# Kernel optimization log

Hardware: AMD Instinct MI355X
Metric: run time of the kernel (lower is better)

Reference implementation:

```python
import jax, jax.numpy as jnp
import numpy as np

T, B, D, H = 512, 64, 512, 512  # seq_len, batch, input_size, hidden_size


def setup_inputs() -> dict:
    key = jax.random.key(0)
    ks = jax.random.split(key, 7)
    s = jnp.float32(0.05)  # keep gates out of saturation
    return {
        "x": jax.random.normal(ks[0], (T, B, D), jnp.float32),
        "Wi_l0": jax.random.normal(ks[1], (2, 4 * H, D), jnp.float32) * s,
        "Wh_l0": jax.random.normal(ks[2], (2, 4 * H, H), jnp.float32) * s,
        "b_l0": jax.random.normal(ks[3], (2, 4 * H), jnp.float32) * s,
        "Wi_l1": jax.random.normal(ks[4], (2, 4 * H, 2 * H), jnp.float32) * s,
        "Wh_l1": jax.random.normal(ks[5], (2, 4 * H, H), jnp.float32) * s,
        "b_l1": jax.random.normal(ks[6], (2, 4 * H), jnp.float32) * s,
    }


def _lstm_dir(xs, Wi, Wh, b):
    """Run one LSTM direction over xs: [T, B, Din] -> ([T, B, H], h_T, c_T)."""
    Bsz = xs.shape[1]
    Hh = Wh.shape[-1]
    # Precompute input contribution for all timesteps (the big GEMM).
    gx = jnp.einsum('tbd,gd->tbg', xs, Wi) + b  # [T, B, 4H]

    def step(carry, gx_t):
        h, c = carry
        gates = gx_t + h @ Wh.T  # [B, 4H]
        i, f, g, o = jnp.split(gates, 4, axis=-1)
        c = jax.nn.sigmoid(f) * c + jax.nn.sigmoid(i) * jnp.tanh(g)
        h = jax.nn.sigmoid(o) * jnp.tanh(c)
        return (h, c), h

    h0 = jnp.zeros((Bsz, Hh), xs.dtype)
    (hT, cT), hs = jax.lax.scan(step, (h0, h0), gx)
    return hs, hT, cT


def _bilstm_layer(xs, Wi, Wh, b):
    hf, hTf, cTf = _lstm_dir(xs, Wi[0], Wh[0], b[0])
    hb, hTb, cTb = _lstm_dir(xs[::-1], Wi[1], Wh[1], b[1])
    # torch.stack(dim=2).view(T, B, -1) == concat along feature axis
    out = jnp.concatenate([hf, hb[::-1]], axis=-1)  # [T, B, 2H]
    return out, (hTf, hTb), (cTf, cTb)


def reference(x, Wi_l0, Wh_l0, b_l0, Wi_l1, Wh_l1, b_l1):
    o0, h0s, c0s = _bilstm_layer(x, Wi_l0, Wh_l0, b_l0)
    o1, h1s, c1s = _bilstm_layer(o0, Wi_l1, Wh_l1, b_l1)
    # state order: (layer0 fwd, layer0 bwd, layer1 fwd, layer1 bwd)
    h_n = jnp.stack(h0s + h1s, axis=0)  # [4, B, H]
    c_n = jnp.stack(c0s + c1s, axis=0)  # [4, B, H]
    return o1, (h_n, c_n)
```

## Files before the change

kernel.cpp:

```cpp
#include <hip/hip_runtime.h>
#include <stdint.h>


#define TT 512
#define BATCH 64
#define HH 512
#define NWG 64
#define NCOLS 32

typedef __attribute__((ext_vector_type(8))) short vshort8;
typedef __attribute__((ext_vector_type(4))) float vfloat4;

__device__ __forceinline__ vfloat4 mfma16(vshort8 a, vshort8 b, vfloat4 c) {
    return __builtin_amdgcn_mfma_f32_16x16x32_bf16(a, b, c, 0, 0, 0);
}

__device__ __forceinline__ float sigmoidf_(float x) {
    return 1.f / (1.f + __expf(-x));
}
__device__ __forceinline__ float tanhf_(float x) {
    float e = __expf(2.f * x);
    return 1.f - 2.f / (e + 1.f);
}
__device__ __forceinline__ unsigned short f2bf(float f) {
    uint32_t u = __float_as_uint(f);
    uint32_t r = (u + 0x7fffu + ((u >> 16) & 1u)) >> 16;
    return (unsigned short)r;
}

__global__ void cvt_f32_bf16(const float* __restrict__ src,
                             unsigned short* __restrict__ dst, int n) {
    int i = (blockIdx.x * blockDim.x + threadIdx.x) * 4;
    if (i + 3 < n) {
        float4 v = *(const float4*)(src + i);
        uint2 p;
        p.x = (uint32_t)f2bf(v.x) | ((uint32_t)f2bf(v.y) << 16);
        p.y = (uint32_t)f2bf(v.z) | ((uint32_t)f2bf(v.w) << 16);
        *(uint2*)(dst + i) = p;
    }
}

template <int DIN, bool WRITE_BF16>
__launch_bounds__(256, 1)
__global__ void lstm_phase(const unsigned short* __restrict__ A,
                           const unsigned short* __restrict__ Wi,
                           const unsigned short* __restrict__ Wh,
                           const float* __restrict__ bias,
                           unsigned short* __restrict__ hbuf,
                           int* __restrict__ flags,
                           unsigned short* __restrict__ obf,
                           float* __restrict__ of32,
                           float* __restrict__ hn,
                           float* __restrict__ cn)
{
    __shared__ unsigned short Wlds[NCOLS * DIN];

    const int tid = threadIdx.x;
    const int dir = blockIdx.x >> 6;
    const int wg = blockIdx.x & 63;
    const int j0 = wg * 8;
    const int lane = tid & 63;
    const int wave = tid >> 6;

    for (int chunk = tid; chunk < NCOLS * DIN / 8; chunk += 256) {
        int n = chunk / (DIN / 8);
        int k8 = (chunk % (DIN / 8)) * 8;
        int grow = (n >> 3) * HH + j0 + (n & 7);
        vshort8 v = *(const vshort8*)(Wi + ((size_t)dir * 4 * HH + grow) * DIN + k8);
        int byte = n * DIN * 2 + ((k8 * 2) ^ ((n & 7) << 4));
        *(vshort8*)((char*)Wlds + byte) = v;
    }
    __syncthreads();

    const int arow = wave * 16 + (lane & 15);
    const int kOff = (lane >> 4) * 8;
    const int klane = (lane >> 4) * 16;
    const int n0 = lane & 15;
    const int swz = (n0 & 7) << 4;
    const int nb0 = n0 * DIN * 2;
    const int nb1 = (16 + n0) * DIN * 2;
    const int grow0 = (n0 >> 3) * HH + j0 + (n0 & 7);
    const int grow1 = ((n0 >> 3) + 2) * HH + j0 + (n0 & 7);
    const float bias0 = bias[dir * 4 * HH + grow0];
    const float bias1 = bias[dir * 4 * HH + grow1];
    const bool lo = (lane & 8) == 0;
    const int j = lane & 7;
    const int jcol = j0 + j;
    const int hrowb = wave * 16 + ((lane >> 4) << 2);

    const unsigned short* whp0 = Wh + ((size_t)dir * 4 * HH + grow0) * HH + kOff;
    const unsigned short* whp1 = Wh + ((size_t)dir * 4 * HH + grow1) * HH + kOff;
    vshort8 wh0r[16], wh1r[16];
#pragma unroll
    for (int kk = 0; kk < 16; ++kk) {
        wh0r[kk] = *(const vshort8*)(whp0 + kk * 32);
        wh1r[kk] = *(const vshort8*)(whp1 + kk * 32);
    }

    float cstate[4] = {0.f, 0.f, 0.f, 0.f};

    for (int s = 0; s < TT; ++s) {
        const int t = dir ? (TT - 1 - s) : s;

        vfloat4 acc0, acc1;
        acc0[0] = acc0[1] = acc0[2] = acc0[3] = bias0;
        acc1[0] = acc1[1] = acc1[2] = acc1[3] = bias1;

        const unsigned short* ap = A + ((size_t)t * BATCH + arow) * DIN + kOff;
#pragma unroll 8
        for (int kk = 0; kk < DIN / 32; ++kk) {
            vshort8 a = *(const vshort8*)(ap + kk * 32);
            int kb = kk * 64 + klane;
            vshort8 b0 = *(const vshort8*)((const char*)Wlds + nb0 + (kb ^ swz));
            vshort8 b1 = *(const vshort8*)((const char*)Wlds + nb1 + (kb ^ swz));
            acc0 = mfma16(a, b0, acc0);
            acc1 = mfma16(a, b1, acc1);
        }

        if (s > 0) {
            const int* slotp = flags + ((dir * NWG + lane) << 2) + wave;
            for (;;) {
                int v;
                asm volatile(
                    "global_load_dword %0, %1, off sc0 sc1\n\t"
                    "s_waitcnt vmcnt(0)"
                    : "=v"(v) : "v"(slotp) : "memory");
                if (!__any(v < s)) break;
            }

            const unsigned short* hp =
                hbuf + (((dir << 1) | ((s - 1) & 1)) * BATCH + arow) * HH + kOff;
            vshort8 ha[16];
#pragma unroll
            for (int kk = 0; kk < 16; ++kk)
                asm volatile("global_load_dwordx4 %0, %1, off sc0 sc1"
                             : "=v"(ha[kk]) : "v"(hp + kk * 32) : "memory");
            asm volatile("s_waitcnt vmcnt(0)" ::: "memory");
            __builtin_amdgcn_sched_barrier(0);
#pragma unroll
            for (int kk = 0; kk < 16; ++kk) {
                acc0 = mfma16(ha[kk], wh0r[kk], acc0);
                acc1 = mfma16(ha[kk], wh1r[kk], acc1);
            }
        }

        float hval[4];
#pragma unroll
        for (int r = 0; r < 4; ++r) {
            float own0 = acc0[r], own1 = acc1[r];
            float oth0 = __shfl_xor(own0, 8, 64);
            float oth1 = __shfl_xor(own1, 8, 64);
            float iv = lo ? own0 : oth0;
            float fv = lo ? oth0 : own0;
            float gv = lo ? own1 : oth1;
            float ov = lo ? oth1 : own1;
            float cnew = sigmoidf_(fv) * cstate[r] + sigmoidf_(iv) * tanhf_(gv);
            cstate[r] = cnew;
            hval[r] = sigmoidf_(ov) * tanhf_(cnew);
        }

        unsigned short* hw = hbuf + (size_t)(((dir << 1) | (s & 1)) * BATCH) * HH;
        const int rA = lo ? 0 : 2;
#pragma unroll
        for (int q = 0; q < 2; ++q) {
            int r = rA + q, row = hrowb + r;
            unsigned short hb = f2bf(hval[r]);
            unsigned short* hwp = hw + row * HH + jcol;
            uint32_t hb32 = hb;
            asm volatile("global_store_short %0, %1, off sc0 sc1"
                         :: "v"(hwp), "v"(hb32) : "memory");
            if constexpr (WRITE_BF16)
                obf[((size_t)t * BATCH + row) * (2 * HH) + dir * HH + jcol] = hb;
            else
                of32[((size_t)t * BATCH + row) * (2 * HH) + dir * HH + jcol] = hval[r];
        }
        if (s == TT - 1) {
#pragma unroll
            for (int q = 0; q < 2; ++q) {
                int r = rA + q, row = hrowb + r;
                hn[(dir * BATCH + row) * HH + jcol] = hval[r];
                cn[(dir * BATCH + row) * HH + jcol] = cstate[r];
            }
        }

        asm volatile("s_waitcnt vmcnt(0)" ::: "memory");
        __builtin_amdgcn_sched_barrier(0);
        if (lane == 0) {
            int* myslot = flags + ((dir * NWG + wg) << 2) + wave;
            int ep = s + 1;
            asm volatile("global_store_dword %0, %1, off sc0 sc1"
                         :: "v"(myslot), "v"(ep) : "memory");
        }
    }
}

extern "C" void kernel_launch(void* const* d_in, const int* in_sizes, int n_in,
                              void* d_out, int out_size, void* d_ws, size_t ws_size,
                              hipStream_t stream) {
    const float* x = (const float*)d_in[0];
    const float* Wi0 = (const float*)d_in[1];
    const float* Wh0 = (const float*)d_in[2];
    const float* b0 = (const float*)d_in[3];
    const float* Wi1 = (const float*)d_in[4];
    const float* Wh1 = (const float*)d_in[5];
    const float* b1 = (const float*)d_in[6];

    char* ws = (char*)d_ws;
    int* flags = (int*)(ws + 0);
    unsigned short* hbuf = (unsigned short*)(ws + 8192);
    unsigned short* wi0b = (unsigned short*)(ws + 270336);
    unsigned short* wh0b = (unsigned short*)(ws + 4464640);
    unsigned short* wi1b = (unsigned short*)(ws + 8658944);
    unsigned short* wh1b = (unsigned short*)(ws + 17047552);
    unsigned short* xb = (unsigned short*)(ws + 21241856);
    unsigned short* o0 = (unsigned short*)(ws + 54796288);

    float* out = (float*)d_out;
    const size_t O1SZ = (size_t)TT * BATCH * 2 * HH;
    float* hn_base = out + O1SZ;
    float* cn_base = out + O1SZ + 4 * BATCH * HH;

    hipMemsetAsync(flags, 0, 4096, stream);

    {
        int n;
        n = TT * BATCH * 512;
        cvt_f32_bf16<<<n / 1024, 256, 0, stream>>>(x, xb, n);
        n = 2 * 2048 * 512;
        cvt_f32_bf16<<<n / 1024, 256, 0, stream>>>(Wi0, wi0b, n);
        cvt_f32_bf16<<<n / 1024, 256, 0, stream>>>(Wh0, wh0b, n);
        cvt_f32_bf16<<<n / 1024, 256, 0, stream>>>(Wh1, wh1b, n);
        n = 2 * 2048 * 1024;
        cvt_f32_bf16<<<n / 1024, 256, 0, stream>>>(Wi1, wi1b, n);
    }

    lstm_phase<512, true><<<128, 256, 0, stream>>>(
        xb, wi0b, wh0b, b0, hbuf, flags, o0, nullptr, hn_base, cn_base);

    lstm_phase<1024, false><<<128, 256, 0, stream>>>(
        o0, wi1b, wh1b, b1, hbuf, flags + 512, nullptr, out,
        hn_base + 2 * BATCH * HH, cn_base + 2 * BATCH * HH);
}
```

Before: 8.543 ms.

## Replace per-workgroup flag polling with atomic counters and convert Wh in-kernel

Swaps the per-workgroup epoch flags, which each wave polled across 64 lanes, for a single atomic counter per direction and wave. The consumer polls one cache line with readfirstlane, backing off with s_sleep. The producer now increments the counter right after its h stores, before writing the output, so that write leaves the critical path. It also drops the separate Wh bf16 conversion kernels by converting fp32 weights to bf16 in registers at kernel start. LDS is padded to the maximum size, which looks like a way to force one workgroup per CU. The trade-offs are atomic contention on a shared counter and sleep latency added to each step.

```diff
diff --git a/kernel.cpp b/kernel.cpp
--- a/kernel.cpp
+++ b/kernel.cpp
@@ -44,18 +44,21 @@
 __launch_bounds__(256, 1)
 __global__ void lstm_phase(const unsigned short* __restrict__ A,
                            const unsigned short* __restrict__ Wi,
-                           const unsigned short* __restrict__ Wh,
+                           const float* __restrict__ Whf,
                            const float* __restrict__ bias,
                            unsigned short* __restrict__ hbuf,
-                           int* __restrict__ flags,
+                           uint32_t* __restrict__ cnt,
                            unsigned short* __restrict__ obf,
                            float* __restrict__ of32,
                            float* __restrict__ hn,
                            float* __restrict__ cn)
 {
-    __shared__ unsigned short Wlds[NCOLS * DIN];
+    __shared__ unsigned short Wlds[NCOLS * 1024];
+    __shared__ unsigned short Wpad[16 * 1024];
 
     const int tid = threadIdx.x;
+    ((volatile unsigned short*)Wpad)[tid] = 0;
+
     const int dir = blockIdx.x >> 6;
     const int wg = blockIdx.x & 63;
     const int j0 = wg * 8;
@@ -84,17 +87,31 @@
     const float bias0 = bias[dir * 4 * HH + grow0];
     const float bias1 = bias[dir * 4 * HH + grow1];
     const bool lo = (lane & 8) == 0;
-    const int j = lane & 7;
-    const int jcol = j0 + j;
+    const int jcol = j0 + (lane & 7);
     const int hrowb = wave * 16 + ((lane >> 4) << 2);
-
-    const unsigned short* whp0 = Wh + ((size_t)dir * 4 * HH + grow0) * HH + kOff;
-    const unsigned short* whp1 = Wh + ((size_t)dir * 4 * HH + grow1) * HH + kOff;
+    uint32_t* const cline = cnt + (dir * 4 + wave) * 32;
+
+    const float* whf0 = Whf + ((size_t)dir * 4 * HH + grow0) * HH + kOff;
+    const float* whf1 = Whf + ((size_t)dir * 4 * HH + grow1) * HH + kOff;
     vshort8 wh0r[16], wh1r[16];
 #pragma unroll
     for (int kk = 0; kk < 16; ++kk) {
-        wh0r[kk] = *(const vshort8*)(whp0 + kk * 32);
-        wh1r[kk] = *(const vshort8*)(whp1 + kk * 32);
+        float4 a0 = *(const float4*)(whf0 + kk * 32);
+        float4 a1 = *(const float4*)(whf0 + kk * 32 + 4);
+        float4 b0 = *(const float4*)(whf1 + kk * 32);
+        float4 b1 = *(const float4*)(whf1 + kk * 32 + 4);
+        vshort8 a, b;
+        a[0] = (short)f2bf(a0.x); a[1] = (short)f2bf(a0.y);
+        a[2] = (short)f2bf(a0.z); a[3] = (short)f2bf(a0.w);
+        a[4] = (short)f2bf(a1.x); a[5] = (short)f2bf(a1.y);
+        a[6] = (short)f2bf(a1.z); a[7] = (short)f2bf(a1.w);
+        b[0] = (short)f2bf(b0.x); b[1] = (short)f2bf(b0.y);
+        b[2] = (short)f2bf(b0.z); b[3] = (short)f2bf(b0.w);
+        b[4] = (short)f2bf(b1.x); b[5] = (short)f2bf(b1.y);
+        b[6] = (short)f2bf(b1.z); b[7] = (short)f2bf(b1.w);
+        wh0r[kk] = a;
+        wh1r[kk] = b;
+        asm volatile("" : "+v"(wh0r[kk]), "+v"(wh1r[kk]));
     }
 
     float cstate[4] = {0.f, 0.f, 0.f, 0.f};
@@ -118,29 +135,31 @@
         }
 
         if (s > 0) {
-            const int* slotp = flags + ((dir * NWG + lane) << 2) + wave;
+            const uint32_t target = 64u * (uint32_t)s;
             for (;;) {
-                int v;
+                uint32_t v;
                 asm volatile(
                     "global_load_dword %0, %1, off sc0 sc1\n\t"
                     "s_waitcnt vmcnt(0)"
-                    : "=v"(v) : "v"(slotp) : "memory");
-                if (!__any(v < s)) break;
+                    : "=v"(v) : "v"(cline) : "memory");
+                if (__builtin_amdgcn_readfirstlane(v) >= target) break;
+                __builtin_amdgcn_s_sleep(1);
             }
+            __builtin_amdgcn_sched_barrier(0);
 
             const unsigned short* hp =
                 hbuf + (((dir << 1) | ((s - 1) & 1)) * BATCH + arow) * HH + kOff;
-            vshort8 ha[16];
+            vshort8 hd[16];
 #pragma unroll
             for (int kk = 0; kk < 16; ++kk)
                 asm volatile("global_load_dwordx4 %0, %1, off sc0 sc1"
-                             : "=v"(ha[kk]) : "v"(hp + kk * 32) : "memory");
+                             : "=v"(hd[kk]) : "v"(hp + kk * 32));
             asm volatile("s_waitcnt vmcnt(0)" ::: "memory");
             __builtin_amdgcn_sched_barrier(0);
 #pragma unroll
             for (int kk = 0; kk < 16; ++kk) {
-                acc0 = mfma16(ha[kk], wh0r[kk], acc0);
-                acc1 = mfma16(ha[kk], wh1r[kk], acc1);
+                acc0 = mfma16(hd[kk], wh0r[kk], acc0);
+                acc1 = mfma16(hd[kk], wh1r[kk], acc1);
             }
         }
 
@@ -161,18 +180,29 @@
 
         unsigned short* hw = hbuf + (size_t)(((dir << 1) | (s & 1)) * BATCH) * HH;
         const int rA = lo ? 0 : 2;
+        unsigned short hb[2];
+        hb[0] = f2bf(hval[rA]);
+        hb[1] = f2bf(hval[rA + 1]);
 #pragma unroll
         for (int q = 0; q < 2; ++q) {
-            int r = rA + q, row = hrowb + r;
-            unsigned short hb = f2bf(hval[r]);
-            unsigned short* hwp = hw + row * HH + jcol;
-            uint32_t hb32 = hb;
+            int row = hrowb + rA + q;
+            unsigned short* wp = hw + row * HH + jcol;
+            uint32_t v32 = hb[q];
             asm volatile("global_store_short %0, %1, off sc0 sc1"
-                         :: "v"(hwp), "v"(hb32) : "memory");
+                         :: "v"(wp), "v"(v32) : "memory");
+        }
+        asm volatile("s_waitcnt vmcnt(0)" ::: "memory");
+        __builtin_amdgcn_sched_barrier(0);
+        if (lane == 0) atomicAdd((unsigned int*)cline, 1u);
+
+#pragma unroll
+        for (int q = 0; q < 2; ++q) {
+            int row = hrowb + rA + q;
             if constexpr (WRITE_BF16)
-                obf[((size_t)t * BATCH + row) * (2 * HH) + dir * HH + jcol] = hb;
+                obf[((size_t)t * BATCH + row) * (2 * HH) + dir * HH + jcol] = hb[q];
             else
-                of32[((size_t)t * BATCH + row) * (2 * HH) + dir * HH + jcol] = hval[r];
+                of32[((size_t)t * BATCH + row) * (2 * HH) + dir * HH + jcol] =
+                    hval[q == 0 ? rA : rA + 1];
         }
         if (s == TT - 1) {
 #pragma unroll
@@ -181,15 +211,6 @@
                 hn[(dir * BATCH + row) * HH + jcol] = hval[r];
                 cn[(dir * BATCH + row) * HH + jcol] = cstate[r];
             }
-        }
-
-        asm volatile("s_waitcnt vmcnt(0)" ::: "memory");
-        __builtin_amdgcn_sched_barrier(0);
-        if (lane == 0) {
-            int* myslot = flags + ((dir * NWG + wg) << 2) + wave;
-            int ep = s + 1;
-            asm volatile("global_store_dword %0, %1, off sc0 sc1"
-                         :: "v"(myslot), "v"(ep) : "memory");
         }
     }
 }
@@ -206,21 +227,21 @@
     const float* b1 = (const float*)d_in[6];
 
     char* ws = (char*)d_ws;
-    int* flags = (int*)(ws + 0);
-    unsigned short* hbuf = (unsigned short*)(ws + 8192);
-    unsigned short* wi0b = (unsigned short*)(ws + 270336);
-    unsigned short* wh0b = (unsigned short*)(ws + 4464640);
-    unsigned short* wi1b = (unsigned short*)(ws + 8658944);
-    unsigned short* wh1b = (unsigned short*)(ws + 17047552);
-    unsigned short* xb = (unsigned short*)(ws + 21241856);
-    unsigned short* o0 = (unsigned short*)(ws + 54796288);
+    uint32_t* cntA = (uint32_t*)(ws);
+    uint32_t* cntB = (uint32_t*)(ws + 2048);
+    unsigned short* hbufA = (unsigned short*)(ws + 8192);
+    unsigned short* hbufB = (unsigned short*)(ws + 270336);
+    unsigned short* wi0b = (unsigned short*)(ws + 1048576);
+    unsigned short* wi1b = (unsigned short*)(ws + 5242880);
+    unsigned short* xb = (unsigned short*)(ws + 13631488);
+    unsigned short* o0 = (unsigned short*)(ws + 47185920);
 
     float* out = (float*)d_out;
     const size_t O1SZ = (size_t)TT * BATCH * 2 * HH;
     float* hn_base = out + O1SZ;
     float* cn_base = out + O1SZ + 4 * BATCH * HH;
 
-    hipMemsetAsync(flags, 0, 4096, stream);
+    hipMemsetAsync(ws, 0, 4096, stream);
 
     {
         int n;
@@ -228,16 +249,14 @@
         cvt_f32_bf16<<<n / 1024, 256, 0, stream>>>(x, xb, n);
         n = 2 * 2048 * 512;
         cvt_f32_bf16<<<n / 1024, 256, 0, stream>>>(Wi0, wi0b, n);
-        cvt_f32_bf16<<<n / 1024, 256, 0, stream>>>(Wh0, wh0b, n);
-        cvt_f32_bf16<<<n / 1024, 256, 0, stream>>>(Wh1, wh1b, n);
         n = 2 * 2048 * 1024;
         cvt_f32_bf16<<<n / 1024, 256, 0, stream>>>(Wi1, wi1b, n);
     }
 
     lstm_phase<512, true><<<128, 256, 0, stream>>>(
-        xb, wi0b, wh0b, b0, hbuf, flags, o0, nullptr, hn_base, cn_base);
+        xb, wi0b, Wh0, b0, hbufA, cntA, o0, nullptr, hn_base, cn_base);
 
     lstm_phase<1024, false><<<128, 256, 0, stream>>>(
-        o0, wi1b, wh1b, b1, hbuf, flags + 512, nullptr, out,
+        o0, wi1b, Wh1, b1, hbufB, cntB, nullptr, out,
         hn_base + 2 * BATCH * HH, cn_base + 2 * BATCH * HH);
 }
```

Result: faster. 7.380 ms (-13.6%).
